# Optimization experiments

Measured on AMD Instinct MI355X. Metric: run time of the kernel, lower is better.

The kernel has to match this reference:

```python
import jax, jax.numpy as jnp
import numpy as np

N = 25600      # nodes
DEG = 16       # incoming edges per node
E = N * DEG    # 409600 edges
B = 8          # graphs in batch
F = 7          # node features
H = 300        # hidden_channels
L = 100        # latent_channels


def _mlp(h, W1, b1, W2, b2, W3, b3):
    h = jax.nn.relu(h @ W1 + b1)
    h = jax.nn.relu(h @ W2 + b2)
    return h @ W3 + b3


def _edge_layer(x, src, dst, params):
    # PyG MessagePassing(aggr='max'), flow source_to_target:
    # x_j = x[src] (edge_index[0]), x_i = x[dst] (edge_index[1])
    x_i = x[dst]
    x_j = x[src]
    m = _mlp(jnp.concatenate([x_i, x_j - x_i], axis=-1), *params)  # [E, out]
    # every node has >=1 incoming edge by construction, so no empty segments
    return jax.ops.segment_max(m, dst, num_segments=x.shape[0])


def setup_inputs() -> dict:
    key = jax.random.key(0)
    ks = jax.random.split(key, 24)
    x = jax.random.normal(ks[0], (N, F), jnp.float32)
    dst = jnp.repeat(jnp.arange(N, dtype=jnp.int32), DEG)          # every node covered
    src = jax.random.randint(ks[1], (E,), 0, N, dtype=jnp.int32)
    edge_index = jnp.stack([src, dst])                              # [2, E]
    batch = jnp.repeat(jnp.arange(B, dtype=jnp.int32), N // B)     # sorted graph ids

    def lin(k, i, o):
        return jax.random.normal(k, (i, o), jnp.float32) / jnp.sqrt(jnp.float32(i))

    def bias(k, o):
        return jax.random.normal(k, (o,), jnp.float32) * 0.01

    inp = dict(x=x, edge_index=edge_index, batch=batch)
    # layer 0 MLP: 2*F -> H -> H -> L
    inp.update(l0_W1=lin(ks[2], 2 * F, H), l0_b1=bias(ks[3], H),
               l0_W2=lin(ks[4], H, H),     l0_b2=bias(ks[5], H),
               l0_W3=lin(ks[6], H, L),     l0_b3=bias(ks[7], L))
    # layer 1 MLP: 2*L -> H -> H -> L
    inp.update(l1_W1=lin(ks[8], 2 * L, H), l1_b1=bias(ks[9], H),
               l1_W2=lin(ks[10], H, H),    l1_b2=bias(ks[11], H),
               l1_W3=lin(ks[12], H, L),    l1_b3=bias(ks[13], L))
    # final lin: 3*L -> L -> L -> 1
    inp.update(lin_W1=lin(ks[14], 3 * L, L), lin_b1=bias(ks[15], L),
               lin_W2=lin(ks[16], L, L),     lin_b2=bias(ks[17], L),
               lin_W3=lin(ks[18], L, 1),     lin_b3=bias(ks[19], 1))
    return inp


def reference(x, edge_index, batch,
              l0_W1, l0_b1, l0_W2, l0_b2, l0_W3, l0_b3,
              l1_W1, l1_b1, l1_W2, l1_b2, l1_W3, l1_b3,
              lin_W1, lin_b1, lin_W2, lin_b2, lin_W3, lin_b3):
    src, dst = edge_index[0], edge_index[1]
    h = _edge_layer(x, src, dst, (l0_W1, l0_b1, l0_W2, l0_b2, l0_W3, l0_b3))
    h = jax.nn.relu(h)
    h = _edge_layer(h, src, dst, (l1_W1, l1_b1, l1_W2, l1_b2, l1_W3, l1_b3))
    h = jax.nn.relu(h)                                              # [N, L]
    addp = jax.ops.segment_sum(h, batch, num_segments=B)
    cnt = jax.ops.segment_sum(jnp.ones((h.shape[0], 1), h.dtype), batch, num_segments=B)
    meanp = addp / cnt
    maxp = jax.ops.segment_max(h, batch, num_segments=B)
    pooled = jnp.concatenate([addp, meanp, maxp], axis=1)           # [B, 3L]
    return _mlp(pooled, lin_W1, lin_b1, lin_W2, lin_b2, lin_W3, lin_b3)  # [B, 1]
```

## Files before the change

kernel.cpp:

```cpp
#include <hip/hip_runtime.h>

#define NNODES 25600
#define DEG 16
#define BGRAPHS 8
#define NPG (NNODES / BGRAPHS)
#define FDIM 7
#define HDIM 300
#define LDIM 100
#define HP 320
#define UVW 640
#define NT1 20
#define KS1 10
#define NT2 7
#define KS2 10
#define H0W 128
#define SSTR 328

typedef __attribute__((ext_vector_type(8))) _Float16 half8;
typedef __attribute__((ext_vector_type(2))) _Float16 half2v;
typedef __attribute__((ext_vector_type(4))) float floatx4;

__device__ __forceinline__ unsigned short f2h(float f) {
    _Float16 h = (_Float16)f;
    return __builtin_bit_cast(unsigned short, h);
}

__device__ __forceinline__ half2v pkrtz(float a, float b) {
    return __builtin_bit_cast(half2v, __builtin_amdgcn_cvt_pkrtz(a, b));
}

union UV4H { uint4 v; half2v h[4]; };

__device__ __forceinline__ unsigned short packB(const float* W, int Kreal, int Nreal,
                                                int KS, int rel)
{
    int j = rel & 7, lane = (rel >> 3) & 63, rem = rel >> 9;
    int ks = rem % KS, nt = rem / KS;
    int k = ks * 32 + ((lane >> 4) << 3) + j;
    int n = nt * 16 + (lane & 15);
    float v = (k < Kreal && n < Nreal) ? W[k * Nreal + n] : 0.f;
    return f2h(v);
}

__device__ __forceinline__ unsigned short packProjW(const float* W1, int Ksub,
                                                    int KS, int rel)
{
    int j = rel & 7, lane = (rel >> 3) & 63, rem = rel >> 9;
    int ks = rem % KS, nt = rem / KS;
    int k = ks * 32 + ((lane >> 4) << 3) + j;
    int n = nt * 16 + (lane & 15);
    float v = 0.f;
    if (k < Ksub) {
        if (n < HP) { if (n < HDIM) v = W1[k * HDIM + n] - W1[(k + Ksub) * HDIM + n]; }
        else { int m = n - HP; if (m < HDIM) v = W1[(k + Ksub) * HDIM + m]; }
    }
    return f2h(v);
}

#define S0 102400
#define S1 102400
#define S2 35840
#define S3 35840
#define S4 81920
#define S5 20480
#define S6 1920
#define S7 40000
#define PACK_TOTAL (S0+S1+S2+S3+S4+S5+S6+S7)

__global__ __launch_bounds__(256) void pack_all_kernel(
    const float* __restrict__ l0_W1, const float* __restrict__ l0_b1,
    const float* __restrict__ l0_W2, const float* __restrict__ l0_b2,
    const float* __restrict__ l0_W3,
    const float* __restrict__ l1_W1, const float* __restrict__ l1_b1,
    const float* __restrict__ l1_W2, const float* __restrict__ l1_b2,
    const float* __restrict__ l1_W3,
    unsigned short* __restrict__ PB2_0, unsigned short* __restrict__ PB2_1,
    unsigned short* __restrict__ PB3_0, unsigned short* __restrict__ PB3_1,
    unsigned short* __restrict__ PW1,  unsigned short* __restrict__ PW0,
    float* __restrict__ b2p_0, float* __restrict__ b2p_1,
    float* __restrict__ bp1,   float* __restrict__ bp0,
    float* __restrict__ part)
{
    int idx = blockIdx.x * 256 + threadIdx.x;
    if (idx >= PACK_TOTAL) return;
    if (idx < S0) { PB2_0[idx] = packB(l0_W2, HDIM, HDIM, KS1, idx); return; }
    idx -= S0;
    if (idx < S1) { PB2_1[idx] = packB(l1_W2, HDIM, HDIM, KS1, idx); return; }
    idx -= S1;
    if (idx < S2) { PB3_0[idx] = packB(l0_W3, HDIM, LDIM, KS2, idx); return; }
    idx -= S2;
    if (idx < S3) { PB3_1[idx] = packB(l1_W3, HDIM, LDIM, KS2, idx); return; }
    idx -= S3;
    if (idx < S4) { PW1[idx] = packProjW(l1_W1, LDIM, 4, idx); return; }
    idx -= S4;
    if (idx < S5) { PW0[idx] = packProjW(l0_W1, FDIM, 1, idx); return; }
    idx -= S5;
    if (idx < 320)       { b2p_0[idx] = (idx < HDIM) ? l0_b2[idx] : 0.f; return; }
    if (idx < 640)       { int n = idx - 320; b2p_1[n] = (n < HDIM) ? l1_b2[n] : 0.f; return; }
    if (idx < 1280)      { int n = idx - 640; bp1[n] = (n < HDIM) ? l1_b1[n] : 0.f; return; }
    if (idx < 1920)      { int n = idx - 1280; bp0[n] = (n < HDIM) ? l0_b1[n] : 0.f; return; }
    part[idx - 1920] = 0.f;
}

template<int KS, bool A_IS_X>
__global__ __launch_bounds__(256) void proj_gemm_kernel(
    const void* __restrict__ Asrc, const unsigned short* __restrict__ PW,
    const float* __restrict__ bp,
    unsigned short* __restrict__ UV)
{
    __shared__ unsigned short As[4 * KS * 64 * 8];
    __shared__ unsigned short S[64 * SSTR];
    const int t = threadIdx.x;
    const int row0 = blockIdx.x * 64;

    if constexpr (A_IS_X) {
        const float* x = (const float*)Asrc;
        int lane = t & 63, mt = t >> 6;
        int quad = lane >> 4;
        int grow = row0 + mt * 16 + (lane & 15);
        unsigned short oz[8];
#pragma unroll
        for (int j = 0; j < 8; ++j) {
            int k = quad * 8 + j;
            oz[j] = (k < FDIM) ? f2h(x[grow * FDIM + k]) : (unsigned short)0;
        }
        *(uint4*)(As + t * 8) = *(uint4*)oz;
    } else {
        const unsigned short* h = (const unsigned short*)Asrc;
#pragma unroll
        for (int i = 0; i < 4; ++i) {
            int s = t + 256 * i;
            int lane = s & 63;
            int ks = (s >> 6) % KS;
            int mt = s / (KS * 64);
            int grow = row0 + mt * 16 + (lane & 15);
            int k0 = ks * 32 + ((lane >> 4) << 3);
            *(uint4*)(As + s * 8) = *(const uint4*)(h + (size_t)grow * H0W + k0);
        }
    }
    __syncthreads();

    const int w = t >> 6, lane = t & 63, quad = lane >> 4, l15 = lane & 15;

    for (int g = 0; g < 2; ++g) {
        const int ntb = g * 20 + w * 5;
        floatx4 c[5][4];
#pragma unroll
        for (int i = 0; i < 5; ++i)
#pragma unroll
            for (int mt = 0; mt < 4; ++mt) c[i][mt] = (floatx4){0.f, 0.f, 0.f, 0.f};
#pragma unroll
        for (int ks = 0; ks < KS; ++ks) {
            half8 a[4];
#pragma unroll
            for (int mt = 0; mt < 4; ++mt)
                a[mt] = *(const half8*)(As + ((mt * KS + ks) * 64 + lane) * 8);
#pragma unroll
            for (int i = 0; i < 5; ++i) {
                half8 b = *(const half8*)(PW + (size_t)(((ntb + i) * KS + ks) * 64 + lane) * 8);
#pragma unroll
                for (int mt = 0; mt < 4; ++mt)
                    c[i][mt] = __builtin_amdgcn_mfma_f32_16x16x32_f16(a[mt], b, c[i][mt], 0, 0, 0);
            }
        }
        __syncthreads();
#pragma unroll
        for (int i = 0; i < 5; ++i) {
            int colp = (w * 5 + i) * 16 + l15;
            float bb = bp[g * 320 + colp];
#pragma unroll
            for (int mt = 0; mt < 4; ++mt) {
#pragma unroll
                for (int r = 0; r < 4; ++r) {
                    int row = mt * 16 + quad * 4 + r;
                    S[row * SSTR + colp] = f2h(c[i][mt][r] + bb);
                }
            }
        }
        __syncthreads();
#pragma unroll
        for (int it = 0; it < 10; ++it) {
            int s = t + 256 * it;
            int row = s / 40, c4 = s - row * 40;
            uint4 v = *(const uint4*)(S + row * SSTR + c4 * 8);
            *(uint4*)(UV + (size_t)(row0 + row) * UVW + g * 320 + c4 * 8) = v;
        }
    }
}

template<bool OUT_HALF>
__global__ __launch_bounds__(512, 4) void edge_mfma_kernel(
    const unsigned short* __restrict__ UV,
    const int* __restrict__ src,
    const unsigned short* __restrict__ PB2, const float* __restrict__ b2p,
    const unsigned short* __restrict__ PB3, const float* __restrict__ b3,
    void* __restrict__ hout)
{
    __shared__ unsigned short Zs[4 * KS1 * 64 * 8];

    const int t = threadIdx.x;
    const int node0 = blockIdx.x * 4;
    const int lane = t & 63;
    const int w = t >> 6;
    const int quad = lane >> 4;
    const int l15 = lane & 15;
    const int slane = lane ^ ((lane & 0x30) >> 3);

    const int row16 = lane >> 2;
    const int part  = lane & 3;
    const int fl    = row16 + 16 * part;
    const int phys  = fl ^ (part << 1);

    const half2v hzero = {(_Float16)0.f, (_Float16)0.f};

#pragma unroll
    for (int i = 0; i < 5; ++i) {
        int s = t + 512 * i;
        int ks = (s >> 6) % KS1;
        int mt = s / (KS1 * 64);
        int m = mt * 16 + row16;
        int k0 = ks * 32 + part * 8;
        int srcn = src[node0 * 16 + m];
        UV4H ud, vd, o;
        ud.v = *(const uint4*)(UV + (size_t)(node0 + mt) * UVW + k0);
        vd.v = *(const uint4*)(UV + (size_t)srcn * UVW + HP + k0);
#pragma unroll
        for (int d = 0; d < 4; ++d) {
            half2v s2 = ud.h[d] + vd.h[d];
            o.h[d] = __builtin_elementwise_max(s2, hzero);
        }
        *(uint4*)(Zs + ((mt * KS1 + ks) * 64 + phys) * 8) = o.v;
    }
    __syncthreads();

    const int cnt1  = (w < 4) ? 3 : 2;
    const int base1 = (w < 4) ? 3 * w : 12 + 2 * (w - 4);
    floatx4 c1[3][4];
#pragma unroll
    for (int i = 0; i < 3; ++i)
#pragma unroll
        for (int mt = 0; mt < 4; ++mt) c1[i][mt] = (floatx4){0.f, 0.f, 0.f, 0.f};
    for (int ks = 0; ks < KS1; ++ks) {
        half8 zb[4];
#pragma unroll
        for (int mt = 0; mt < 4; ++mt)
            zb[mt] = *(const half8*)(Zs + ((mt * KS1 + ks) * 64 + slane) * 8);
#pragma unroll
        for (int i = 0; i < 3; ++i) {
            if (i < cnt1) {
                half8 wa = *(const half8*)(PB2 + (size_t)(((base1 + i) * KS1 + ks) * 64 + lane) * 8);
#pragma unroll
                for (int mt = 0; mt < 4; ++mt)
                    c1[i][mt] = __builtin_amdgcn_mfma_f32_16x16x32_f16(wa, zb[mt], c1[i][mt], 0, 0, 0);
            }
        }
    }
    __syncthreads();

#pragma unroll
    for (int i = 0; i < 3; ++i) {
        if (i < cnt1) {
            int B = base1 + i;
            const floatx4 bb = *(const floatx4*)(b2p + B * 16 + quad * 4);
            half2v hb0 = pkrtz(bb[0], bb[1]);
            half2v hb1 = pkrtz(bb[2], bb[3]);
            int ks = B >> 1;
            int khi = (2 * B + (quad >> 1)) & 3;
            int jo = (quad & 1) * 4;
#pragma unroll
            for (int mt = 0; mt < 4; ++mt) {
                half2v c01 = pkrtz(c1[i][mt][0], c1[i][mt][1]);
                half2v c23 = pkrtz(c1[i][mt][2], c1[i][mt][3]);
                union { half2v h[2]; unsigned long long ll; } o;
                o.h[0] = __builtin_elementwise_max(c01 + hb0, hzero);
                o.h[1] = __builtin_elementwise_max(c23 + hb1, hzero);
                *(unsigned long long*)(Zs + ((mt * KS1 + ks) * 64 + l15 + 16 * khi) * 8 + jo) = o.ll;
            }
        }
    }
    __syncthreads();

    floatx4 c2[4];
#pragma unroll
    for (int mt = 0; mt < 4; ++mt) c2[mt] = (floatx4){0.f, 0.f, 0.f, 0.f};
    if (w < NT2) {
        for (int ks = 0; ks < KS2; ++ks) {
            half8 a[4];
#pragma unroll
            for (int mt = 0; mt < 4; ++mt)
                a[mt] = *(const half8*)(Zs + ((mt * KS2 + ks) * 64 + lane) * 8);
            half8 b = *(const half8*)(PB3 + (size_t)((w * KS2 + ks) * 64 + lane) * 8);
#pragma unroll
            for (int mt = 0; mt < 4; ++mt)
                c2[mt] = __builtin_amdgcn_mfma_f32_16x16x32_f16(a[mt], b, c2[mt], 0, 0, 0);
        }
    }

    if constexpr (OUT_HALF) {
#pragma unroll
        for (int mt = 0; mt < 4; ++mt) {
            int node = node0 + mt;
            if (w < NT2) {
                int col = w * 16 + l15;
                floatx4 a = c2[mt];
                float mx = fmaxf(fmaxf(a[0], a[1]), fmaxf(a[2], a[3]));
                mx = fmaxf(mx, __shfl_xor(mx, 16, 64));
                mx = fmaxf(mx, __shfl_xor(mx, 32, 64));
                if (quad == 0) {
                    unsigned short val = 0;
                    if (col < LDIM) val = f2h(fmaxf(mx + b3[col], 0.f));
                    ((unsigned short*)hout)[(size_t)node * H0W + col] = val;
                }
            }
            if (w == 7 && quad == 0)
                ((unsigned short*)hout)[(size_t)node * H0W + 112 + l15] = 0;
        }
    } else {
        if (w < NT2) {
            int col = w * 16 + l15;
            float bv = (col < LDIM) ? b3[col] : 0.f;
            float s4 = 0.f, m4 = 0.f;
#pragma unroll
            for (int mt = 0; mt < 4; ++mt) {
                floatx4 a = c2[mt];
                float mx = fmaxf(fmaxf(a[0], a[1]), fmaxf(a[2], a[3]));
                mx = fmaxf(mx, __shfl_xor(mx, 16, 64));
                mx = fmaxf(mx, __shfl_xor(mx, 32, 64));
                float v = fmaxf(mx + bv, 0.f);
                s4 += v;
                m4 = fmaxf(m4, v);
            }
            if (quad == 0 && col < LDIM) {
                int slice = blockIdx.x >> 5;
                float* ps = (float*)hout + (size_t)slice * 200;
                atomicAdd(ps + col, s4);
                atomicMax((int*)(ps + 100 + col), __float_as_int(m4));
            }
        }
    }
}

__global__ __launch_bounds__(256) void final_kernel(
    const float* __restrict__ part,
    const float* __restrict__ W1, const float* __restrict__ b1,
    const float* __restrict__ W2, const float* __restrict__ b2,
    const float* __restrict__ W3, const float* __restrict__ b3,
    float* __restrict__ out)
{
    __shared__ float P[BGRAPHS][3 * LDIM];
    __shared__ float T1[BGRAPHS][LDIM];
    __shared__ float T2[BGRAPHS][LDIM];
    int t = threadIdx.x;
    for (int i = t; i < BGRAPHS * LDIM; i += 256) {
        int g = i / LDIM, f = i - (i / LDIM) * LDIM;
        float s = 0.f, mx = 0.f;
        for (int sl = 0; sl < 25; ++sl) {
            s += part[(size_t)(g * 25 + sl) * 200 + f];
            mx = fmaxf(mx, part[(size_t)(g * 25 + sl) * 200 + 100 + f]);
        }
        P[g][f] = s;
        P[g][LDIM + f] = s * (1.0f / NPG);
        P[g][2 * LDIM + f] = mx;
    }
    __syncthreads();
    for (int i = t; i < BGRAPHS * LDIM; i += 256) {
        int g = i / LDIM, c = i - (i / LDIM) * LDIM;
        float a = b1[c];
        for (int k = 0; k < 3 * LDIM; ++k) a = fmaf(P[g][k], W1[k * LDIM + c], a);
        T1[g][c] = fmaxf(a, 0.f);
    }
    __syncthreads();
    for (int i = t; i < BGRAPHS * LDIM; i += 256) {
        int g = i / LDIM, c = i - (i / LDIM) * LDIM;
        float a = b2[c];
        for (int k = 0; k < LDIM; ++k) a = fmaf(T1[g][k], W2[k * LDIM + c], a);
        T2[g][c] = fmaxf(a, 0.f);
    }
    __syncthreads();
    if (t < BGRAPHS) {
        float a = b3[0];
        for (int k = 0; k < LDIM; ++k) a = fmaf(T2[t][k], W3[k], a);
        out[t] = a;
    }
}

extern "C" void kernel_launch(void* const* d_in, const int* in_sizes, int n_in,
                              void* d_out, int out_size, void* d_ws, size_t ws_size,
                              hipStream_t stream)
{
    const float* x      = (const float*)d_in[0];
    const int*   src    = (const int*)d_in[1];
    const float* l0_W1  = (const float*)d_in[3];
    const float* l0_b1  = (const float*)d_in[4];
    const float* l0_W2  = (const float*)d_in[5];
    const float* l0_b2  = (const float*)d_in[6];
    const float* l0_W3  = (const float*)d_in[7];
    const float* l0_b3  = (const float*)d_in[8];
    const float* l1_W1  = (const float*)d_in[9];
    const float* l1_b1  = (const float*)d_in[10];
    const float* l1_W2  = (const float*)d_in[11];
    const float* l1_b2  = (const float*)d_in[12];
    const float* l1_W3  = (const float*)d_in[13];
    const float* l1_b3  = (const float*)d_in[14];
    const float* lin_W1 = (const float*)d_in[15];
    const float* lin_b1 = (const float*)d_in[16];
    const float* lin_W2 = (const float*)d_in[17];
    const float* lin_b2 = (const float*)d_in[18];
    const float* lin_W3 = (const float*)d_in[19];
    const float* lin_b3 = (const float*)d_in[20];
    float* out = (float*)d_out;

    char* p = (char*)d_ws;
    unsigned short* UV    = (unsigned short*)p;  p += (size_t)NNODES * UVW * 2;
    unsigned short* h0b   = (unsigned short*)p;  p += (size_t)NNODES * H0W * 2;
    unsigned short* PB2_0 = (unsigned short*)p;  p += (size_t)S0 * 2;
    unsigned short* PB2_1 = (unsigned short*)p;  p += (size_t)S1 * 2;
    unsigned short* PB3_0 = (unsigned short*)p;  p += (size_t)S2 * 2;
    unsigned short* PB3_1 = (unsigned short*)p;  p += (size_t)S3 * 2;
    unsigned short* PW1   = (unsigned short*)p;  p += (size_t)S4 * 2;
    unsigned short* PW0   = (unsigned short*)p;  p += (size_t)S5 * 2;
    float* b2p_0          = (float*)p;           p += HP * 4;
    float* b2p_1          = (float*)p;           p += HP * 4;
    float* bp1            = (float*)p;           p += 640 * 4;
    float* bp0            = (float*)p;           p += 640 * 4;
    float* part           = (float*)p;           p += (size_t)200 * 200 * 4;

    pack_all_kernel<<<(PACK_TOTAL + 255) / 256, 256, 0, stream>>>(
        l0_W1, l0_b1, l0_W2, l0_b2, l0_W3,
        l1_W1, l1_b1, l1_W2, l1_b2, l1_W3,
        PB2_0, PB2_1, PB3_0, PB3_1, PW1, PW0, b2p_0, b2p_1, bp1, bp0, part);

    proj_gemm_kernel<1, true><<<NNODES / 64, 256, 0, stream>>>(x, PW0, bp0, UV);
    edge_mfma_kernel<true><<<NNODES / 4, 512, 0, stream>>>(UV, src, PB2_0, b2p_0, PB3_0, l0_b3, h0b);
    proj_gemm_kernel<4, false><<<NNODES / 64, 256, 0, stream>>>(h0b, PW1, bp1, UV);
    edge_mfma_kernel<false><<<NNODES / 4, 512, 0, stream>>>(UV, src, PB2_1, b2p_1, PB3_1, l1_b3, part);
    final_kernel<<<1, 256, 0, stream>>>(part, lin_W1, lin_b1, lin_W2, lin_b2, lin_W3, lin_b3, out);
}
```

Baseline: 420.0 us.

## Split projection GEMM halves across blocks and rebalance edge MLP tile assignment

```diff
diff --git a/kernel.cpp b/kernel.cpp
--- a/kernel.cpp
+++ b/kernel.cpp
@@ -111,7 +111,8 @@
     __shared__ unsigned short As[4 * KS * 64 * 8];
     __shared__ unsigned short S[64 * SSTR];
     const int t = threadIdx.x;
-    const int row0 = blockIdx.x * 64;
+    const int g = blockIdx.x & 1;
+    const int row0 = (blockIdx.x >> 1) * 64;
 
     if constexpr (A_IS_X) {
         const float* x = (const float*)Asrc;
@@ -141,50 +142,47 @@
     __syncthreads();
 
     const int w = t >> 6, lane = t & 63, quad = lane >> 4, l15 = lane & 15;
-
-    for (int g = 0; g < 2; ++g) {
-        const int ntb = g * 20 + w * 5;
-        floatx4 c[5][4];
-#pragma unroll
-        for (int i = 0; i < 5; ++i)
-#pragma unroll
-            for (int mt = 0; mt < 4; ++mt) c[i][mt] = (floatx4){0.f, 0.f, 0.f, 0.f};
-#pragma unroll
-        for (int ks = 0; ks < KS; ++ks) {
-            half8 a[4];
+    const int ntb = g * 20 + w * 5;
+
+    floatx4 c[5][4];
+#pragma unroll
+    for (int i = 0; i < 5; ++i)
+#pragma unroll
+        for (int mt = 0; mt < 4; ++mt) c[i][mt] = (floatx4){0.f, 0.f, 0.f, 0.f};
+#pragma unroll
+    for (int ks = 0; ks < KS; ++ks) {
+        half8 a[4];
+#pragma unroll
+        for (int mt = 0; mt < 4; ++mt)
+            a[mt] = *(const half8*)(As + ((mt * KS + ks) * 64 + lane) * 8);
+#pragma unroll
+        for (int i = 0; i < 5; ++i) {
+            half8 b = *(const half8*)(PW + (size_t)(((ntb + i) * KS + ks) * 64 + lane) * 8);
 #pragma unroll
             for (int mt = 0; mt < 4; ++mt)
-                a[mt] = *(const half8*)(As + ((mt * KS + ks) * 64 + lane) * 8);
-#pragma unroll
-            for (int i = 0; i < 5; ++i) {
-                half8 b = *(const half8*)(PW + (size_t)(((ntb + i) * KS + ks) * 64 + lane) * 8);
-#pragma unroll
-                for (int mt = 0; mt < 4; ++mt)
-                    c[i][mt] = __builtin_amdgcn_mfma_f32_16x16x32_f16(a[mt], b, c[i][mt], 0, 0, 0);
+                c[i][mt] = __builtin_amdgcn_mfma_f32_16x16x32_f16(a[mt], b, c[i][mt], 0, 0, 0);
+        }
+    }
+#pragma unroll
+    for (int i = 0; i < 5; ++i) {
+        int colp = (w * 5 + i) * 16 + l15;
+        float bb = bp[g * 320 + colp];
+#pragma unroll
+        for (int mt = 0; mt < 4; ++mt) {
+#pragma unroll
+            for (int r = 0; r < 4; ++r) {
+                int row = mt * 16 + quad * 4 + r;
+                S[row * SSTR + colp] = f2h(c[i][mt][r] + bb);
             }
         }
-        __syncthreads();
-#pragma unroll
-        for (int i = 0; i < 5; ++i) {
-            int colp = (w * 5 + i) * 16 + l15;
-            float bb = bp[g * 320 + colp];
-#pragma unroll
-            for (int mt = 0; mt < 4; ++mt) {
-#pragma unroll
-                for (int r = 0; r < 4; ++r) {
-                    int row = mt * 16 + quad * 4 + r;
-                    S[row * SSTR + colp] = f2h(c[i][mt][r] + bb);
-                }
-            }
-        }
-        __syncthreads();
-#pragma unroll
-        for (int it = 0; it < 10; ++it) {
-            int s = t + 256 * it;
-            int row = s / 40, c4 = s - row * 40;
-            uint4 v = *(const uint4*)(S + row * SSTR + c4 * 8);
-            *(uint4*)(UV + (size_t)(row0 + row) * UVW + g * 320 + c4 * 8) = v;
-        }
+    }
+    __syncthreads();
+#pragma unroll
+    for (int it = 0; it < 10; ++it) {
+        int s = t + 256 * it;
+        int row = s / 40, c4 = s - row * 40;
+        uint4 v = *(const uint4*)(S + row * SSTR + c4 * 8);
+        *(uint4*)(UV + (size_t)(row0 + row) * UVW + g * 320 + c4 * 8) = v;
     }
 }
 
@@ -233,50 +231,72 @@
     }
     __syncthreads();
 
-    const int cnt1  = (w < 4) ? 3 : 2;
-    const int base1 = (w < 4) ? 3 * w : 12 + 2 * (w - 4);
-    floatx4 c1[3][4];
-#pragma unroll
-    for (int i = 0; i < 3; ++i)
-#pragma unroll
-        for (int mt = 0; mt < 4; ++mt) c1[i][mt] = (floatx4){0.f, 0.f, 0.f, 0.f};
-    for (int ks = 0; ks < KS1; ++ks) {
-        half8 zb[4];
-#pragma unroll
-        for (int mt = 0; mt < 4; ++mt)
-            zb[mt] = *(const half8*)(Zs + ((mt * KS1 + ks) * 64 + slane) * 8);
-#pragma unroll
-        for (int i = 0; i < 3; ++i) {
-            if (i < cnt1) {
-                half8 wa = *(const half8*)(PB2 + (size_t)(((base1 + i) * KS1 + ks) * 64 + lane) * 8);
-#pragma unroll
-                for (int mt = 0; mt < 4; ++mt)
-                    c1[i][mt] = __builtin_amdgcn_mfma_f32_16x16x32_f16(wa, zb[mt], c1[i][mt], 0, 0, 0);
-            }
-        }
-    }
-    __syncthreads();
-
-#pragma unroll
-    for (int i = 0; i < 3; ++i) {
-        if (i < cnt1) {
-            int B = base1 + i;
-            const floatx4 bb = *(const floatx4*)(b2p + B * 16 + quad * 4);
-            half2v hb0 = pkrtz(bb[0], bb[1]);
-            half2v hb1 = pkrtz(bb[2], bb[3]);
-            int ks = B >> 1;
-            int khi = (2 * B + (quad >> 1)) & 3;
-            int jo = (quad & 1) * 4;
-#pragma unroll
-            for (int mt = 0; mt < 4; ++mt) {
-                half2v c01 = pkrtz(c1[i][mt][0], c1[i][mt][1]);
-                half2v c23 = pkrtz(c1[i][mt][2], c1[i][mt][3]);
-                union { half2v h[2]; unsigned long long ll; } o;
-                o.h[0] = __builtin_elementwise_max(c01 + hb0, hzero);
-                o.h[1] = __builtin_elementwise_max(c23 + hb1, hzero);
-                *(unsigned long long*)(Zs + ((mt * KS1 + ks) * 64 + l15 + 16 * khi) * 8 + jo) = o.ll;
-            }
-        }
+    const int B0 = (5 * w) >> 1;
+    floatx4 c1[5][2];
+#pragma unroll
+    for (int j = 0; j < 5; ++j) {
+        c1[j][0] = (floatx4){0.f, 0.f, 0.f, 0.f};
+        c1[j][1] = (floatx4){0.f, 0.f, 0.f, 0.f};
+    }
+    const unsigned short* pb = PB2 + (size_t)B0 * (KS1 * 512) + lane * 8;
+
+#define MM(A, B, C) __builtin_amdgcn_mfma_f32_16x16x32_f16((A), (B), (C), 0, 0, 0)
+    if ((w & 1) == 0) {
+        for (int ks = 0; ks < KS1; ++ks) {
+            half8 zb[4];
+#pragma unroll
+            for (int mt = 0; mt < 4; ++mt)
+                zb[mt] = *(const half8*)(Zs + ((mt * KS1 + ks) * 64 + slane) * 8);
+            half8 wa0 = *(const half8*)(pb + (0 * KS1 + ks) * 512);
+            half8 wa1 = *(const half8*)(pb + (1 * KS1 + ks) * 512);
+            half8 wa2 = *(const half8*)(pb + (2 * KS1 + ks) * 512);
+            c1[0][0] = MM(wa0, zb[0], c1[0][0]); c1[0][1] = MM(wa0, zb[1], c1[0][1]);
+            c1[1][0] = MM(wa0, zb[2], c1[1][0]); c1[1][1] = MM(wa0, zb[3], c1[1][1]);
+            c1[2][0] = MM(wa1, zb[0], c1[2][0]); c1[2][1] = MM(wa1, zb[1], c1[2][1]);
+            c1[3][0] = MM(wa1, zb[2], c1[3][0]); c1[3][1] = MM(wa1, zb[3], c1[3][1]);
+            c1[4][0] = MM(wa2, zb[0], c1[4][0]); c1[4][1] = MM(wa2, zb[1], c1[4][1]);
+        }
+    } else {
+        for (int ks = 0; ks < KS1; ++ks) {
+            half8 zb[4];
+#pragma unroll
+            for (int mt = 0; mt < 4; ++mt)
+                zb[mt] = *(const half8*)(Zs + ((mt * KS1 + ks) * 64 + slane) * 8);
+            half8 wa0 = *(const half8*)(pb + (0 * KS1 + ks) * 512);
+            half8 wa1 = *(const half8*)(pb + (1 * KS1 + ks) * 512);
+            half8 wa2 = *(const half8*)(pb + (2 * KS1 + ks) * 512);
+            c1[0][0] = MM(wa0, zb[2], c1[0][0]); c1[0][1] = MM(wa0, zb[3], c1[0][1]);
+            c1[1][0] = MM(wa1, zb[0], c1[1][0]); c1[1][1] = MM(wa1, zb[1], c1[1][1]);
+            c1[2][0] = MM(wa1, zb[2], c1[2][0]); c1[2][1] = MM(wa1, zb[3], c1[2][1]);
+            c1[3][0] = MM(wa2, zb[0], c1[3][0]); c1[3][1] = MM(wa2, zb[1], c1[3][1]);
+            c1[4][0] = MM(wa2, zb[2], c1[4][0]); c1[4][1] = MM(wa2, zb[3], c1[4][1]);
+        }
+    }
+#undef MM
+    __syncthreads();
+
+    auto z2u = [&](int j, int Bt, int h) {
+        const floatx4 bb = *(const floatx4*)(b2p + Bt * 16 + quad * 4);
+        half2v hb0 = pkrtz(bb[0], bb[1]);
+        half2v hb1 = pkrtz(bb[2], bb[3]);
+        int ksq = Bt >> 1;
+        int khi = (2 * Bt + (quad >> 1)) & 3;
+        int jo = (quad & 1) * 4;
+#pragma unroll
+        for (int m2 = 0; m2 < 2; ++m2) {
+            int mt = 2 * h + m2;
+            half2v c01 = pkrtz(c1[j][m2][0], c1[j][m2][1]);
+            half2v c23 = pkrtz(c1[j][m2][2], c1[j][m2][3]);
+            union { half2v hh[2]; unsigned long long ll; } o;
+            o.hh[0] = __builtin_elementwise_max(c01 + hb0, hzero);
+            o.hh[1] = __builtin_elementwise_max(c23 + hb1, hzero);
+            *(unsigned long long*)(Zs + ((mt * KS1 + ksq) * 64 + l15 + 16 * khi) * 8 + jo) = o.ll;
+        }
+    };
+    if ((w & 1) == 0) {
+        z2u(0, B0, 0); z2u(1, B0, 1); z2u(2, B0 + 1, 0); z2u(3, B0 + 1, 1); z2u(4, B0 + 2, 0);
+    } else {
+        z2u(0, B0, 1); z2u(1, B0 + 1, 0); z2u(2, B0 + 1, 1); z2u(3, B0 + 2, 0); z2u(4, B0 + 2, 1);
     }
     __syncthreads();
 
@@ -430,9 +450,9 @@
         l1_W1, l1_b1, l1_W2, l1_b2, l1_W3,
         PB2_0, PB2_1, PB3_0, PB3_1, PW1, PW0, b2p_0, b2p_1, bp1, bp0, part);
 
-    proj_gemm_kernel<1, true><<<NNODES / 64, 256, 0, stream>>>(x, PW0, bp0, UV);
+    proj_gemm_kernel<1, true><<<NNODES / 32, 256, 0, stream>>>(x, PW0, bp0, UV);
     edge_mfma_kernel<true><<<NNODES / 4, 512, 0, stream>>>(UV, src, PB2_0, b2p_0, PB3_0, l0_b3, h0b);
-    proj_gemm_kernel<4, false><<<NNODES / 64, 256, 0, stream>>>(h0b, PW1, bp1, UV);
+    proj_gemm_kernel<4, false><<<NNODES / 32, 256, 0, stream>>>(h0b, PW1, bp1, UV);
     edge_mfma_kernel<false><<<NNODES / 4, 512, 0, stream>>>(UV, src, PB2_1, b2p_1, PB3_1, l1_b3, part);
     final_kernel<<<1, 256, 0, stream>>>(part, lin_W1, lin_b1, lin_W2, lin_b2, lin_W3, lin_b3, out);
 }
```

Result: slower. 432.6 us (+3.0%).
